# Performance work log

Hardware: AMD Instinct MI355X
Metric: run time of the kernel (lower is better)

The kernel has to match this reference:

```python
import jax, jax.numpy as jnp
import numpy as np

B, E, H, V, T = 64, 512, 1024, 30000, 20
START = 1  # vocab['<start>']


def setup_inputs() -> dict:
    key = jax.random.key(0)
    ks = jax.random.split(key, 12)
    s = 0.05  # small init so log_softmax/tanh stay well-conditioned
    return {
        "encoded_image": jax.random.normal(ks[0], (B, E), jnp.float32),
        "Wemb": jax.random.normal(ks[1], (V, E), jnp.float32) * s,
        "Wih1": jax.random.normal(ks[2], (4 * H, 2 * E), jnp.float32) * s,
        "Whh1": jax.random.normal(ks[3], (4 * H, H), jnp.float32) * s,
        "bih1": jax.random.normal(ks[4], (4 * H,), jnp.float32) * s,
        "bhh1": jax.random.normal(ks[5], (4 * H,), jnp.float32) * s,
        "Wih2": jax.random.normal(ks[6], (4 * H, H), jnp.float32) * s,
        "Whh2": jax.random.normal(ks[7], (4 * H, H), jnp.float32) * s,
        "bih2": jax.random.normal(ks[8], (4 * H,), jnp.float32) * s,
        "bhh2": jax.random.normal(ks[9], (4 * H,), jnp.float32) * s,
        "Wout": jax.random.normal(ks[10], (V, H), jnp.float32) * s,
        "bout": jax.random.normal(ks[11], (V,), jnp.float32) * s,
    }


def _lstm_cell(x, h, c, Wih, Whh, bih, bhh):
    # torch.nn.LSTMCell: gates in (i, f, g, o) row order
    g = x @ Wih.T + bih + h @ Whh.T + bhh
    i, f, gg, o = jnp.split(g, 4, axis=-1)
    c_new = jax.nn.sigmoid(f) * c + jax.nn.sigmoid(i) * jnp.tanh(gg)
    h_new = jax.nn.sigmoid(o) * jnp.tanh(c_new)
    return h_new, c_new


def reference(encoded_image, Wemb, Wih1, Whh1, bih1, bhh1,
              Wih2, Whh2, bih2, bhh2, Wout, bout):
    Bn = encoded_image.shape[0]
    dt = encoded_image.dtype
    h1 = c1 = h2 = c2 = jnp.zeros((Bn, H), dt)
    # pre-loop step with zero word embedding
    x0 = jnp.concatenate([encoded_image, jnp.zeros((Bn, E), dt)], axis=-1)
    h1, c1 = _lstm_cell(x0, h1, c1, Wih1, Whh1, bih1, bhh1)
    h2, c2 = _lstm_cell(h1, h2, c2, Wih2, Whh2, bih2, bhh2)
    # output[:, 0] = one_hot(<start>)  (dropout is identity in eval mode)
    row0 = jnp.zeros((Bn, V), dt).at[:, START].set(1.0)
    prev_tok = jnp.full((Bn,), START, jnp.int32)

    def step(carry, _):
        h1, c1, h2, c2, tok = carry
        emb = Wemb[tok]                                   # [B, E] gather
        x = jnp.concatenate([encoded_image, emb], axis=-1)
        h1, c1 = _lstm_cell(x, h1, c1, Wih1, Whh1, bih1, bhh1)
        h2, c2 = _lstm_cell(h1, h2, c2, Wih2, Whh2, bih2, bhh2)
        logp = jax.nn.log_softmax(h2 @ Wout.T + bout, axis=-1)  # [B, V]
        tok = jnp.argmax(logp, axis=-1).astype(jnp.int32)
        return (h1, c1, h2, c2, tok), logp

    _, rows = jax.lax.scan(step, (h1, c1, h2, c2, prev_tok), None, length=T - 1)
    out = jnp.concatenate([row0[:, None, :], jnp.transpose(rows, (1, 0, 2))], axis=1)
    return out  # [B, T, V]
```

## Files before the change

### kernel.cpp

```cpp
#include <hip/hip_runtime.h>
#include <math.h>

#define BB 64
#define EE 512
#define HH 1024
#define VV 30000
#define TT 20
#define NBT 469
#define PSTRIDE 512

typedef __attribute__((ext_vector_type(8))) short bf16x8;
typedef __attribute__((ext_vector_type(4))) float f32x4;

#define OFF_W1  ((size_t)0)
#define OFF_W2  ((size_t)33554432)
#define OFF_WO  ((size_t)67108864)
#define OFF_X1  ((size_t)190054400)
#define OFF_H1  ((size_t)190316544)
#define OFF_H2  ((size_t)190840832)
#define OFF_C1  ((size_t)191365120)
#define OFF_C2  ((size_t)191627264)
#define OFF_P   ((size_t)191889408)
#define OFF_PM  ((size_t)200278016)
#define OFF_PS  ((size_t)200409088)
#define OFF_PA  ((size_t)200540160)
#define OFF_LSE ((size_t)200671232)
#define OFF_BS  ((size_t)200676352)
#define OFF_GX  ((size_t)200709120)

__device__ __forceinline__ unsigned short bf_hi(float x) {
    unsigned u = __float_as_uint(x);
    return (unsigned short)((u + 0x7fffu + ((u >> 16) & 1u)) >> 16);
}
__device__ __forceinline__ float bf_f(unsigned short h) {
    return __uint_as_float(((unsigned)h) << 16);
}
__device__ __forceinline__ void merge3(float& m, float& s, int& a,
                                       float m2, float s2, int a2) {
    if (m2 > m) { s = s * expf(m - m2) + s2; m = m2; a = a2; }
    else if (m2 == m) { s += s2; if (a2 < a) a = a2; }
    else { s += s2 * expf(m2 - m); }
}
__device__ __forceinline__ void gl16(const void* g, void* l) {
    __builtin_amdgcn_global_load_lds(
        (const unsigned int __attribute__((address_space(1)))*)g,
        (unsigned int __attribute__((address_space(3)))*)l, 16, 0, 0);
}
__device__ __forceinline__ void cvt8(const float* src, uint4& hv, uint4& lv) {
    unsigned h[8], q[8];
    #pragma unroll
    for (int i = 0; i < 8; ++i) {
        float x = src[i];
        unsigned short hi = bf_hi(x);
        unsigned short lo = bf_hi(x - bf_f(hi));
        h[i] = hi; q[i] = lo;
    }
    hv.x = h[0] | (h[1] << 16); hv.y = h[2] | (h[3] << 16);
    hv.z = h[4] | (h[5] << 16); hv.w = h[6] | (h[7] << 16);
    lv.x = q[0] | (q[1] << 16); lv.y = q[2] | (q[3] << 16);
    lv.z = q[4] | (q[5] << 16); lv.w = q[6] | (q[7] << 16);
}

__global__ __launch_bounds__(256) void k_conv_cell(
    const float* __restrict__ Wih1, const float* __restrict__ Whh1,
    const float* __restrict__ Wih2, const float* __restrict__ Whh2, char* wsb) {
    int cell = blockIdx.y;
    const float* Wih = cell ? Wih2 : Wih1;
    const float* Whh = cell ? Whh2 : Whh1;
    char* dst = wsb + (cell ? OFF_W2 : OFF_W1);
    unsigned flat = blockIdx.x * 256 + threadIdx.x;
    unsigned c = flat & 511, kt = (flat >> 9) & 31, rt = flat >> 14;
    unsigned s = c >> 8, bg = (c >> 6) & 3, g = (c >> 4) & 3, n = c & 15;
    unsigned row = bg * 1024 + rt * 16 + n;
    unsigned col = (kt & 15) * 64 + s * 32 + g * 8;
    const float* src = (kt < 16 ? Wih : Whh) + (size_t)row * 1024 + col;
    uint4 hv, lv; cvt8(src, hv, lv);
    char* d = dst + (size_t)rt * 524288 + kt * 16384 + c * 16;
    *(uint4*)d = hv;
    *(uint4*)(d + 8192) = lv;
}

__global__ __launch_bounds__(256) void k_conv_out(const float* __restrict__ Wout,
                                                  char* wsb) {
    unsigned flat = blockIdx.x * 256 + threadIdx.x;
    unsigned c = flat & 511, kt = (flat >> 9) & 15, rt = flat >> 13;
    unsigned s = c >> 8, bg = (c >> 6) & 3, g = (c >> 4) & 3, n = c & 15;
    unsigned row = rt * 64 + bg * 16 + n; if (row > VV - 1) row = VV - 1;
    unsigned col = kt * 64 + s * 32 + g * 8;
    const float* src = Wout + (size_t)row * 1024 + col;
    uint4 hv, lv; cvt8(src, hv, lv);
    char* d = wsb + OFF_WO + (size_t)rt * 262144 + kt * 16384 + c * 16;
    *(uint4*)d = hv;
    *(uint4*)(d + 8192) = lv;
}

__global__ __launch_bounds__(256) void k_conv_img(const float* __restrict__ img,
                                                  char* wsb) {
    unsigned flat = blockIdx.x * 256 + threadIdx.x;
    unsigned c = flat & 511, kt = flat >> 9;
    unsigned s = c >> 8, bg = (c >> 6) & 3, g = (c >> 4) & 3, n = c & 15;
    unsigned b = bg * 16 + n;
    unsigned col = kt * 64 + s * 32 + g * 8;
    const float* src = img + (size_t)b * 512 + col;
    uint4 hv, lv; cvt8(src, hv, lv);
    char* d = wsb + OFF_X1 + kt * 16384 + c * 16;
    *(uint4*)d = hv;
    *(uint4*)(d + 8192) = lv;
}

__global__ void k_prep(char* wsb,
                       const float* __restrict__ bih1, const float* __restrict__ bhh1,
                       const float* __restrict__ bih2, const float* __restrict__ bhh2) {
    unsigned idx = blockIdx.x * 256 + threadIdx.x;
    if (idx < 131072) { ((unsigned*)(wsb + OFF_C1))[idx] = 0u; return; }
    idx -= 131072;
    if (idx < 65536) { ((unsigned*)(wsb + OFF_H1))[idx] = 0u; return; }
    idx -= 65536;
    if (idx < 65536) { ((unsigned*)(wsb + OFF_H2))[idx] = 0u; return; }
    idx -= 65536;
    if (idx < 32768) { ((unsigned*)(wsb + OFF_X1 + 131072))[idx] = 0u; return; }
    idx -= 32768;
    if (idx < 8192) {
        float v = (idx < 4096) ? bih1[idx] + bhh1[idx]
                               : bih2[idx - 4096] + bhh2[idx - 4096];
        ((float*)(wsb + OFF_BS))[idx] = v;
    }
}

__device__ __forceinline__ void emb_write(char* X1, const float* Wemb, int tk,
                                          int b, int tid) {
    #pragma unroll
    for (int i = 0; i < 2; ++i) {
        int e = tid + i * 256;
        float x = Wemb[(size_t)tk * 512 + e];
        unsigned short hi = bf_hi(x);
        unsigned short lo = bf_hi(x - bf_f(hi));
        int k = 512 + e;
        int kt = k >> 6, kl = k & 63;
        int s = kl >> 5, gq = (kl >> 3) & 3, off = kl & 7;
        int chunk = s * 256 + (b >> 4) * 64 + gq * 16 + (b & 15);
        char* d = X1 + kt * 16384 + chunk * 16 + off * 2;
        *(unsigned short*)d = hi;
        *(unsigned short*)(d + 8192) = lo;
    }
}

__global__ void k_emb0(const float* __restrict__ Wemb, char* wsb) {
    emb_write(wsb + OFF_X1, Wemb, 1, blockIdx.x, threadIdx.x);
}

template <int NKT>
__device__ __forceinline__ void gemm_core(const char* __restrict__ Wsrc,
                                          const char* __restrict__ A0,
                                          const char* __restrict__ A1,
                                          int ktbase, int HALF,
                                          char* smem, int tid, f32x4 acc[4]) {
    const int l = tid & 63, w = tid >> 6, g = l >> 4, n = l & 15;
    auto stage = [&](int kt, char* buf) {
        const char* wsp = Wsrc + kt * 16384;
        int ta = ktbase + kt;
        const char* asp = (ta < HALF) ? (A0 + ta * 16384)
                                      : (A1 + (ta - HALF) * 16384);
        int o = tid * 16;
        gl16(wsp + o, buf + o);
        gl16(wsp + 4096 + o, buf + 4096 + o);
        gl16(wsp + 8192 + o, buf + 8192 + o);
        gl16(wsp + 12288 + o, buf + 12288 + o);
        gl16(asp + o, buf + 16384 + o);
        gl16(asp + 4096 + o, buf + 20480 + o);
        gl16(asp + 8192 + o, buf + 24576 + o);
        gl16(asp + 12288 + o, buf + 28672 + o);
    };
    stage(0, smem);
    __syncthreads();
    for (int kt = 0; kt < NKT; ++kt) {
        char* buf = smem + (kt & 1) * 32768;
        if (kt + 1 < NKT) stage(kt + 1, smem + ((kt + 1) & 1) * 32768);
        #pragma unroll
        for (int s = 0; s < 2; ++s) {
            int wc = (s * 256 + w * 64 + g * 16 + n) * 16;
            bf16x8 ah = *(const bf16x8*)(buf + wc);
            bf16x8 al = *(const bf16x8*)(buf + 8192 + wc);
            #pragma unroll
            for (int bg = 0; bg < 4; ++bg) {
                int ac = (s * 256 + bg * 64 + g * 16 + n) * 16;
                bf16x8 bh = *(const bf16x8*)(buf + 16384 + ac);
                bf16x8 bl = *(const bf16x8*)(buf + 24576 + ac);
                acc[bg] = __builtin_amdgcn_mfma_f32_16x16x32_bf16(ah, bh, acc[bg], 0, 0, 0);
                acc[bg] = __builtin_amdgcn_mfma_f32_16x16x32_bf16(ah, bl, acc[bg], 0, 0, 0);
                acc[bg] = __builtin_amdgcn_mfma_f32_16x16x32_bf16(al, bh, acc[bg], 0, 0, 0);
            }
        }
        __syncthreads();
    }
}

__global__ __launch_bounds__(256) void k_gximg(char* wsb) {
    __shared__ __align__(16) char smem[65536];
    const int cid = blockIdx.x, tid = threadIdx.x;
    const int l = tid & 63, w = tid >> 6, g = l >> 4, n = l & 15;
    f32x4 acc[4];
    #pragma unroll
    for (int i = 0; i < 4; ++i) acc[i] = (f32x4){0.f, 0.f, 0.f, 0.f};
    gemm_core<8>(wsb + OFF_W1 + (size_t)cid * 524288,
                 wsb + OFF_X1, wsb + OFF_X1, 0, 8, smem, tid, acc);
    const float* bs = (const float*)(wsb + OFF_BS);
    float* gx = (float*)(wsb + OFF_GX) + cid * 4096;
    #pragma unroll
    for (int bg = 0; bg < 4; ++bg)
        #pragma unroll
        for (int p = 0; p < 4; ++p)
            gx[(w * 16 + g * 4 + p) * 64 + bg * 16 + n] =
                acc[bg][p] + bs[w * 1024 + cid * 16 + g * 4 + p];
}

template <int KQT>
__global__ __launch_bounds__(256) void k_cellg(const char* __restrict__ Wbase,
                                               size_t Wskip,
                                               const char* __restrict__ A0,
                                               const char* __restrict__ A1,
                                               int HALF, float* __restrict__ P) {
    __shared__ __align__(16) char smem[65536];
    const int tid = threadIdx.x;
    const int rt = blockIdx.x & 63, kq = blockIdx.x >> 6;
    const char* Wsrc = Wbase + (size_t)rt * 524288 + Wskip + (size_t)kq * KQT * 16384;
    f32x4 acc[4];
    #pragma unroll
    for (int i = 0; i < 4; ++i) acc[i] = (f32x4){0.f, 0.f, 0.f, 0.f};
    gemm_core<KQT>(Wsrc, A0, A1, kq * KQT, HALF, smem, tid, acc);
    const int l = tid & 63, w = tid >> 6, g = l >> 4, n = l & 15;
    float* Pd = P + kq * 262144 + rt * 4096;
    #pragma unroll
    for (int bg = 0; bg < 4; ++bg)
        #pragma unroll
        for (int p = 0; p < 4; ++p)
            Pd[(w * 16 + g * 4 + p) * 64 + bg * 16 + n] = acc[bg][p];
}

__global__ void k_act(const float* __restrict__ P, const float* __restrict__ bs,
                      const float* __restrict__ gx,
                      float* __restrict__ c, char* __restrict__ Hdst) {
    int rt = blockIdx.x, bq = blockIdx.y;
    int jl = threadIdx.x >> 4, bl = threadIdx.x & 15;
    int b = bq * 16 + bl;
    int base = rt * 4096;
    float g4[4];
    #pragma unroll
    for (int gg = 0; gg < 4; ++gg) {
        float v = 0.f;
        #pragma unroll
        for (int kq = 0; kq < 8; ++kq)
            v += P[kq * 262144 + base + (gg * 16 + jl) * 64 + b];
        g4[gg] = v + (gx ? gx[rt * 4096 + gg * 1024 + jl * 64 + b]
                         : bs[gg * 1024 + rt * 16 + jl]);
    }
    float si = 1.f / (1.f + expf(-g4[0]));
    float sf = 1.f / (1.f + expf(-g4[1]));
    float so = 1.f / (1.f + expf(-g4[3]));
    float tg = tanhf(g4[2]);
    int j = rt * 16 + jl;
    int ci = b * 1024 + j;
    float cn = sf * c[ci] + si * tg;
    c[ci] = cn;
    float hn = so * tanhf(cn);
    unsigned short hi = bf_hi(hn);
    unsigned short lo = bf_hi(hn - bf_f(hi));
    int kt = j >> 6, kl = j & 63;
    int s = kl >> 5, gq = (kl >> 3) & 3, off = kl & 7;
    int chunk = s * 256 + (b >> 4) * 64 + gq * 16 + (b & 15);
    char* d = Hdst + kt * 16384 + chunk * 16 + off * 2;
    *(unsigned short*)d = hi;
    *(unsigned short*)(d + 8192) = lo;
}

__global__ __launch_bounds__(256) void k_logits(
    const char* __restrict__ WObase, const float* __restrict__ bout,
    const char* __restrict__ A, float* __restrict__ out, int tstep,
    float* __restrict__ pm, float* __restrict__ ps, int* __restrict__ pa) {
    __shared__ __align__(16) char smem[65536];
    const int tid = threadIdx.x;
    const int v0 = blockIdx.x * 64;
    const char* Wsrc = WObase + (size_t)blockIdx.x * 262144;
    f32x4 acc[4];
    #pragma unroll
    for (int i = 0; i < 4; ++i) acc[i] = (f32x4){0.f, 0.f, 0.f, 0.f};
    gemm_core<16>(Wsrc, A, A, 0, 16, smem, tid, acc);
    const int l = tid & 63, w = tid >> 6, g = l >> 4, n = l & 15;
    int bidx = v0 + w * 16 + g * 4; if (bidx > VV - 4) bidx = VV - 4;
    f32x4 bb4 = *(const f32x4*)&bout[bidx];
    float* gl = (float*)smem;
    #pragma unroll
    for (int bg = 0; bg < 4; ++bg)
        #pragma unroll
        for (int p = 0; p < 4; ++p)
            gl[(bg * 16 + n) * 68 + w * 16 + g * 4 + p] = acc[bg][p] + bb4[p];
    __syncthreads();
    int b = tid >> 2, vq = tid & 3;
    float m = -INFINITY, ssum = 0.f; int am = VV;
    if (v0 + vq * 16 < VV) {
        size_t ob = ((size_t)b * TT + tstep) * VV + v0 + vq * 16;
        #pragma unroll
        for (int e4 = 0; e4 < 4; ++e4) {
            f32x4 vv = *(const f32x4*)&gl[b * 68 + vq * 16 + e4 * 4];
            *(f32x4*)&out[ob + e4 * 4] = vv;
            #pragma unroll
            for (int p = 0; p < 4; ++p)
                merge3(m, ssum, am, vv[p], 1.f, v0 + vq * 16 + e4 * 4 + p);
        }
    }
    #pragma unroll
    for (int off = 1; off < 4; off <<= 1) {
        float m2 = __shfl_xor(m, off, 64);
        float s2 = __shfl_xor(ssum, off, 64);
        int a2 = __shfl_xor(am, off, 64);
        merge3(m, ssum, am, m2, s2, a2);
    }
    if (vq == 0) {
        pm[b * PSTRIDE + blockIdx.x] = m;
        ps[b * PSTRIDE + blockIdx.x] = ssum;
        pa[b * PSTRIDE + blockIdx.x] = am;
    }
}

__global__ void k_reduce(const float* __restrict__ pm, const float* __restrict__ ps,
                         const int* __restrict__ pa, float* __restrict__ lse_all,
                         int t, const float* __restrict__ Wemb, char* __restrict__ X1) {
    int b = blockIdx.x;
    int tid = threadIdx.x;
    float m = -INFINITY, s = 0.f; int a = VV;
    for (int i = tid; i < NBT; i += 256)
        merge3(m, s, a, pm[(size_t)b * PSTRIDE + i], ps[(size_t)b * PSTRIDE + i],
               pa[(size_t)b * PSTRIDE + i]);
    #pragma unroll
    for (int off = 1; off < 64; off <<= 1) {
        float m2 = __shfl_xor(m, off, 64);
        float s2 = __shfl_xor(s, off, 64);
        int   a2 = __shfl_xor(a, off, 64);
        merge3(m, s, a, m2, s2, a2);
    }
    __shared__ float sm[4], ss[4]; __shared__ int sa[4]; __shared__ int stok;
    if ((tid & 63) == 0) { sm[tid >> 6] = m; ss[tid >> 6] = s; sa[tid >> 6] = a; }
    __syncthreads();
    if (tid == 0) {
        for (int w = 1; w < 4; ++w) merge3(m, s, a, sm[w], ss[w], sa[w]);
        lse_all[t * 64 + b] = m + logf(s);
        stok = a;
    }
    __syncthreads();
    emb_write(X1, Wemb, stok, b, tid);
}

__global__ void k_fix(float* __restrict__ out, const float* __restrict__ lse_all) {
    int v4 = blockIdx.x * 256 + threadIdx.x;
    int t = blockIdx.y, b = blockIdx.z;
    if (v4 >= 7500) return;
    size_t o = ((size_t)b * TT + t) * VV + (size_t)v4 * 4;
    f32x4 vv;
    if (t == 0) {
        vv = (f32x4){0.f, 0.f, 0.f, 0.f};
        if (v4 == 0) vv[1] = 1.f;
    } else {
        vv = *(const f32x4*)&out[o];
        float lz = lse_all[t * 64 + b];
        vv[0] -= lz; vv[1] -= lz; vv[2] -= lz; vv[3] -= lz;
    }
    *(f32x4*)&out[o] = vv;
}

extern "C" void kernel_launch(void* const* d_in, const int* in_sizes, int n_in,
                              void* d_out, int out_size, void* d_ws, size_t ws_size,
                              hipStream_t stream) {
    const float* img   = (const float*)d_in[0];
    const float* Wemb  = (const float*)d_in[1];
    const float* Wih1  = (const float*)d_in[2];
    const float* Whh1  = (const float*)d_in[3];
    const float* bih1  = (const float*)d_in[4];
    const float* bhh1  = (const float*)d_in[5];
    const float* Wih2  = (const float*)d_in[6];
    const float* Whh2  = (const float*)d_in[7];
    const float* bih2  = (const float*)d_in[8];
    const float* bhh2  = (const float*)d_in[9];
    const float* Wout  = (const float*)d_in[10];
    const float* bout  = (const float*)d_in[11];
    float* out = (float*)d_out;
    char*  wsb = (char*)d_ws;

    char* W1 = wsb + OFF_W1;
    char* W2 = wsb + OFF_W2;
    char* WO = wsb + OFF_WO;
    char* X1 = wsb + OFF_X1;
    float* c1 = (float*)(wsb + OFF_C1);
    float* c2 = (float*)(wsb + OFF_C2);
    float* P  = (float*)(wsb + OFF_P);
    float* pm = (float*)(wsb + OFF_PM);
    float* ps = (float*)(wsb + OFF_PS);
    int*   pa = (int*)(wsb + OFF_PA);
    float* lse_all = (float*)(wsb + OFF_LSE);
    float* bs = (float*)(wsb + OFF_BS);
    float* gx = (float*)(wsb + OFF_GX);
    auto Hb = [&](size_t base, int bank) { return wsb + base + (size_t)bank * 262144; };

    k_conv_cell<<<dim3(4096, 2), 256, 0, stream>>>(Wih1, Whh1, Wih2, Whh2, wsb);
    k_conv_out<<<15008, 256, 0, stream>>>(Wout, wsb);
    k_conv_img<<<16, 256, 0, stream>>>(img, wsb);
    k_prep<<<1184, 256, 0, stream>>>(wsb, bih1, bhh1, bih2, bhh2);
    k_gximg<<<64, 256, 0, stream>>>(wsb);

    int cur = 0;
    k_cellg<3><<<512, 256, 0, stream>>>(W1, 131072, X1 + 131072, Hb(OFF_H1, cur),
                                        8, P);
    k_emb0<<<64, 256, 0, stream>>>(Wemb, wsb);
    k_act<<<dim3(64, 4), 256, 0, stream>>>(P, bs, gx, c1, Hb(OFF_H1, cur ^ 1));
    k_cellg<4><<<512, 256, 0, stream>>>(W2, 0, Hb(OFF_H1, cur ^ 1), Hb(OFF_H2, cur),
                                        16, P);
    k_act<<<dim3(64, 4), 256, 0, stream>>>(P, bs + 4096, nullptr, c2,
                                           Hb(OFF_H2, cur ^ 1));
    cur = 1;

    for (int t = 1; t < TT; ++t) {
        k_cellg<3><<<512, 256, 0, stream>>>(W1, 131072, X1 + 131072, Hb(OFF_H1, cur),
                                            8, P);
        k_act<<<dim3(64, 4), 256, 0, stream>>>(P, bs, gx, c1, Hb(OFF_H1, cur ^ 1));
        k_cellg<4><<<512, 256, 0, stream>>>(W2, 0, Hb(OFF_H1, cur ^ 1),
                                            Hb(OFF_H2, cur), 16, P);
        k_act<<<dim3(64, 4), 256, 0, stream>>>(P, bs + 4096, nullptr, c2,
                                               Hb(OFF_H2, cur ^ 1));
        k_logits<<<NBT, 256, 0, stream>>>(WO, bout, Hb(OFF_H2, cur ^ 1),
                                          out, t, pm, ps, pa);
        k_reduce<<<64, 256, 0, stream>>>(pm, ps, pa, lse_all, t, Wemb, X1);
        cur ^= 1;
    }
    k_fix<<<dim3(30, TT, BB), 256, 0, stream>>>(out, lse_all);
}
```

Before: 1.184 ms.

## Use single-bf16 Wout for logits and re-rank near-max candidates in fp32

```diff
diff --git a/kernel.cpp b/kernel.cpp
--- a/kernel.cpp
+++ b/kernel.cpp
@@ -27,6 +27,7 @@
 #define OFF_LSE ((size_t)200671232)
 #define OFF_BS  ((size_t)200676352)
 #define OFF_GX  ((size_t)200709120)
+#define OFF_H2F ((size_t)201757696)
 
 __device__ __forceinline__ unsigned short bf_hi(float x) {
     unsigned u = __float_as_uint(x);
@@ -59,6 +60,13 @@
     hv.z = h[4] | (h[5] << 16); hv.w = h[6] | (h[7] << 16);
     lv.x = q[0] | (q[1] << 16); lv.y = q[2] | (q[3] << 16);
     lv.z = q[4] | (q[5] << 16); lv.w = q[6] | (q[7] << 16);
+}
+__device__ __forceinline__ void cvt8hi(const float* src, uint4& hv) {
+    unsigned h[8];
+    #pragma unroll
+    for (int i = 0; i < 8; ++i) h[i] = bf_hi(src[i]);
+    hv.x = h[0] | (h[1] << 16); hv.y = h[2] | (h[3] << 16);
+    hv.z = h[4] | (h[5] << 16); hv.w = h[6] | (h[7] << 16);
 }
 
 __global__ __launch_bounds__(256) void k_conv_cell(
@@ -88,10 +96,9 @@
     unsigned row = rt * 64 + bg * 16 + n; if (row > VV - 1) row = VV - 1;
     unsigned col = kt * 64 + s * 32 + g * 8;
     const float* src = Wout + (size_t)row * 1024 + col;
-    uint4 hv, lv; cvt8(src, hv, lv);
-    char* d = wsb + OFF_WO + (size_t)rt * 262144 + kt * 16384 + c * 16;
+    uint4 hv; cvt8hi(src, hv);
+    char* d = wsb + OFF_WO + (size_t)rt * 131072 + kt * 8192 + c * 16;
     *(uint4*)d = hv;
-    *(uint4*)(d + 8192) = lv;
 }
 
 __global__ __launch_bounds__(256) void k_conv_img(const float* __restrict__ img,
@@ -195,6 +202,44 @@
     }
 }
 
+template <int NKT>
+__device__ __forceinline__ void gemm_core2(const char* __restrict__ Wsrc,
+                                           const char* __restrict__ A,
+                                           char* smem, int tid, f32x4 acc[4]) {
+    const int l = tid & 63, w = tid >> 6, g = l >> 4, n = l & 15;
+    auto stage = [&](int kt, char* buf) {
+        const char* wsp = Wsrc + kt * 8192;
+        const char* asp = A + kt * 16384;
+        int o = tid * 16;
+        gl16(wsp + o, buf + o);
+        gl16(wsp + 4096 + o, buf + 4096 + o);
+        gl16(asp + o, buf + 8192 + o);
+        gl16(asp + 4096 + o, buf + 12288 + o);
+        gl16(asp + 8192 + o, buf + 16384 + o);
+        gl16(asp + 12288 + o, buf + 20480 + o);
+    };
+    stage(0, smem);
+    __syncthreads();
+    for (int kt = 0; kt < NKT; ++kt) {
+        char* buf = smem + (kt & 1) * 24576;
+        if (kt + 1 < NKT) stage(kt + 1, smem + ((kt + 1) & 1) * 24576);
+        #pragma unroll
+        for (int s = 0; s < 2; ++s) {
+            int wc = (s * 256 + w * 64 + g * 16 + n) * 16;
+            bf16x8 wh = *(const bf16x8*)(buf + wc);
+            #pragma unroll
+            for (int bg = 0; bg < 4; ++bg) {
+                int ac = (s * 256 + bg * 64 + g * 16 + n) * 16;
+                bf16x8 ah = *(const bf16x8*)(buf + 8192 + ac);
+                bf16x8 al = *(const bf16x8*)(buf + 16384 + ac);
+                acc[bg] = __builtin_amdgcn_mfma_f32_16x16x32_bf16(wh, ah, acc[bg], 0, 0, 0);
+                acc[bg] = __builtin_amdgcn_mfma_f32_16x16x32_bf16(wh, al, acc[bg], 0, 0, 0);
+            }
+        }
+        __syncthreads();
+    }
+}
+
 __global__ __launch_bounds__(256) void k_gximg(char* wsb) {
     __shared__ __align__(16) char smem[65536];
     const int cid = blockIdx.x, tid = threadIdx.x;
@@ -239,7 +284,8 @@
 
 __global__ void k_act(const float* __restrict__ P, const float* __restrict__ bs,
                       const float* __restrict__ gx,
-                      float* __restrict__ c, char* __restrict__ Hdst) {
+                      float* __restrict__ c, char* __restrict__ Hdst,
+                      float* __restrict__ Hf) {
     int rt = blockIdx.x, bq = blockIdx.y;
     int jl = threadIdx.x >> 4, bl = threadIdx.x & 15;
     int b = bq * 16 + bl;
@@ -263,6 +309,7 @@
     float cn = sf * c[ci] + si * tg;
     c[ci] = cn;
     float hn = so * tanhf(cn);
+    if (Hf) Hf[ci] = hn;
     unsigned short hi = bf_hi(hn);
     unsigned short lo = bf_hi(hn - bf_f(hi));
     int kt = j >> 6, kl = j & 63;
@@ -277,14 +324,14 @@
     const char* __restrict__ WObase, const float* __restrict__ bout,
     const char* __restrict__ A, float* __restrict__ out, int tstep,
     float* __restrict__ pm, float* __restrict__ ps, int* __restrict__ pa) {
-    __shared__ __align__(16) char smem[65536];
+    __shared__ __align__(16) char smem[49152];
     const int tid = threadIdx.x;
     const int v0 = blockIdx.x * 64;
-    const char* Wsrc = WObase + (size_t)blockIdx.x * 262144;
+    const char* Wsrc = WObase + (size_t)blockIdx.x * 131072;
     f32x4 acc[4];
     #pragma unroll
     for (int i = 0; i < 4; ++i) acc[i] = (f32x4){0.f, 0.f, 0.f, 0.f};
-    gemm_core<16>(Wsrc, A, A, 0, 16, smem, tid, acc);
+    gemm_core2<16>(Wsrc, A, smem, tid, acc);
     const int l = tid & 63, w = tid >> 6, g = l >> 4, n = l & 15;
     int bidx = v0 + w * 16 + g * 4; if (bidx > VV - 4) bidx = VV - 4;
     f32x4 bb4 = *(const f32x4*)&bout[bidx];
@@ -324,7 +371,10 @@
 
 __global__ void k_reduce(const float* __restrict__ pm, const float* __restrict__ ps,
                          const int* __restrict__ pa, float* __restrict__ lse_all,
-                         int t, const float* __restrict__ Wemb, char* __restrict__ X1) {
+                         int t, const float* __restrict__ Wemb, char* __restrict__ X1,
+                         const float* __restrict__ out, const float* __restrict__ h2f,
+                         const float* __restrict__ WoutF,
+                         const float* __restrict__ boutF) {
     int b = blockIdx.x;
     int tid = threadIdx.x;
     float m = -INFINITY, s = 0.f; int a = VV;
@@ -338,13 +388,57 @@
         int   a2 = __shfl_xor(a, off, 64);
         merge3(m, s, a, m2, s2, a2);
     }
-    __shared__ float sm[4], ss[4]; __shared__ int sa[4]; __shared__ int stok;
+    __shared__ float sm[4], ss[4]; __shared__ int sa[4];
+    __shared__ float gm;
     if ((tid & 63) == 0) { sm[tid >> 6] = m; ss[tid >> 6] = s; sa[tid >> 6] = a; }
     __syncthreads();
     if (tid == 0) {
-        for (int w = 1; w < 4; ++w) merge3(m, s, a, sm[w], ss[w], sa[w]);
+        for (int wv = 1; wv < 4; ++wv) merge3(m, s, a, sm[wv], ss[wv], sa[wv]);
         lse_all[t * 64 + b] = m + logf(s);
-        stok = a;
+        gm = m;
+    }
+    __syncthreads();
+    __shared__ int cnt; __shared__ int cand[256]; __shared__ float cex[256];
+    __shared__ float pw[4]; __shared__ int stok;
+    if (tid == 0) cnt = 0;
+    __syncthreads();
+    const float* row = out + ((size_t)b * TT + t) * VV;
+    float thr = gm - 0.25f;
+    for (int v4 = tid; v4 < 7500; v4 += 256) {
+        f32x4 vv = *(const f32x4*)&row[v4 * 4];
+        #pragma unroll
+        for (int p = 0; p < 4; ++p)
+            if (vv[p] >= thr) {
+                int idx = atomicAdd(&cnt, 1);
+                if (idx < 256) cand[idx] = v4 * 4 + p;
+            }
+    }
+    __syncthreads();
+    int nc = cnt;
+    if (nc > 256) nc = 0;
+    for (int ci = 0; ci < nc; ++ci) {
+        int v = cand[ci];
+        const float* wr = WoutF + (size_t)v * 1024;
+        const float* hr = h2f + b * 1024;
+        float p4 = 0.f;
+        for (int k = tid; k < 1024; k += 256) p4 += hr[k] * wr[k];
+        #pragma unroll
+        for (int off = 1; off < 64; off <<= 1) p4 += __shfl_xor(p4, off, 64);
+        if ((tid & 63) == 0) pw[tid >> 6] = p4;
+        __syncthreads();
+        if (tid == 0) cex[ci] = pw[0] + pw[1] + pw[2] + pw[3] + boutF[v];
+        __syncthreads();
+    }
+    if (tid == 0) {
+        int best = a;
+        if (nc > 0) {
+            float bm = -INFINITY; best = VV;
+            for (int ci = 0; ci < nc; ++ci) {
+                float e = cex[ci]; int v = cand[ci];
+                if (e > bm || (e == bm && v < best)) { bm = e; best = v; }
+            }
+        }
+        stok = best;
     }
     __syncthreads();
     emb_write(X1, Wemb, stok, b, tid);
@@ -398,6 +492,7 @@
     float* lse_all = (float*)(wsb + OFF_LSE);
     float* bs = (float*)(wsb + OFF_BS);
     float* gx = (float*)(wsb + OFF_GX);
+    float* h2f = (float*)(wsb + OFF_H2F);
     auto Hb = [&](size_t base, int bank) { return wsb + base + (size_t)bank * 262144; };
 
     k_conv_cell<<<dim3(4096, 2), 256, 0, stream>>>(Wih1, Whh1, Wih2, Whh2, wsb);
@@ -410,24 +505,27 @@
     k_cellg<3><<<512, 256, 0, stream>>>(W1, 131072, X1 + 131072, Hb(OFF_H1, cur),
                                         8, P);
     k_emb0<<<64, 256, 0, stream>>>(Wemb, wsb);
-    k_act<<<dim3(64, 4), 256, 0, stream>>>(P, bs, gx, c1, Hb(OFF_H1, cur ^ 1));
+    k_act<<<dim3(64, 4), 256, 0, stream>>>(P, bs, gx, c1, Hb(OFF_H1, cur ^ 1),
+                                           nullptr);
     k_cellg<4><<<512, 256, 0, stream>>>(W2, 0, Hb(OFF_H1, cur ^ 1), Hb(OFF_H2, cur),
                                         16, P);
     k_act<<<dim3(64, 4), 256, 0, stream>>>(P, bs + 4096, nullptr, c2,
-                                           Hb(OFF_H2, cur ^ 1));
+                                           Hb(OFF_H2, cur ^ 1), h2f);
     cur = 1;
 
     for (int t = 1; t < TT; ++t) {
         k_cellg<3><<<512, 256, 0, stream>>>(W1, 131072, X1 + 131072, Hb(OFF_H1, cur),
                                             8, P);
-        k_act<<<dim3(64, 4), 256, 0, stream>>>(P, bs, gx, c1, Hb(OFF_H1, cur ^ 1));
+        k_act<<<dim3(64, 4), 256, 0, stream>>>(P, bs, gx, c1, Hb(OFF_H1, cur ^ 1),
+                                               nullptr);
         k_cellg<4><<<512, 256, 0, stream>>>(W2, 0, Hb(OFF_H1, cur ^ 1),
                                             Hb(OFF_H2, cur), 16, P);
         k_act<<<dim3(64, 4), 256, 0, stream>>>(P, bs + 4096, nullptr, c2,
-                                               Hb(OFF_H2, cur ^ 1));
+                                               Hb(OFF_H2, cur ^ 1), h2f);
         k_logits<<<NBT, 256, 0, stream>>>(WO, bout, Hb(OFF_H2, cur ^ 1),
                                           out, t, pm, ps, pa);
-        k_reduce<<<64, 256, 0, stream>>>(pm, ps, pa, lse_all, t, Wemb, X1);
+        k_reduce<<<64, 256, 0, stream>>>(pm, ps, pa, lse_all, t, Wemb, X1,
+                                         out, h2f, Wout, bout);
         cur ^= 1;
     }
     k_fix<<<dim3(30, TT, BB), 256, 0, stream>>>(out, lse_all);
```

Measured after the change: 3.180 ms. +168.6%, slower.
